# Performance work log

Measured on AMD Instinct MI355X. Metric: run time of the kernel, lower is better.

## Reference

```python
import jax, jax.numpy as jnp
import numpy as np

C = 192; WS = 8; SHIFT = 4; NH = 6; HD = 32; N = WS * WS; EPS = 1e-5


def _cpb_table(ws):
    r = np.arange(-(ws - 1), ws, dtype=np.float32)
    t = np.stack(np.meshgrid(r, r, indexing='ij'), axis=-1) / (ws - 1) * 8.0
    t = np.sign(t) * np.log2(np.abs(t) + 1.0) / np.log2(8.0)
    return t.reshape(-1, 2)  # ((2ws-1)^2, 2)


def _rel_index(ws):
    c = np.stack(np.meshgrid(np.arange(ws), np.arange(ws), indexing='ij')).reshape(2, -1)
    rel = (c[:, :, None] - c[:, None, :]).transpose(1, 2, 0).astype(np.int64)
    rel[..., 0] += ws - 1; rel[..., 1] += ws - 1; rel[..., 0] *= 2 * ws - 1
    return rel.sum(-1)  # (N, N)


def _attn_mask(H, W, ws, shift):
    img = np.zeros((H, W), np.float32); cnt = 0.0
    sl = (slice(0, -ws), slice(-ws, -shift), slice(-shift, None))
    for hs in sl:
        for wsl in sl:
            img[hs, wsl] = cnt; cnt += 1.0
    m = img.reshape(H // ws, ws, W // ws, ws).transpose(0, 2, 1, 3).reshape(-1, ws * ws)
    d = m[:, None, :] - m[:, :, None]
    return np.where(d != 0, -100.0, 0.0).astype(np.float32)  # (nW, N, N)


def _ln(x, g, b):
    mu = jnp.mean(x, -1, keepdims=True)
    var = jnp.mean((x - mu) ** 2, -1, keepdims=True)
    return (x - mu) / jnp.sqrt(var + EPS) * g + b


def setup_inputs() -> dict:
    key = jax.random.key(0)
    ks = jax.random.split(key, 8)
    H = W = 384
    w = lambda k, s: jax.random.normal(k, s, jnp.float32) * 0.05
    return {
        'hidden_states': jax.random.normal(ks[0], (1, H * W, C), jnp.float32),
        'q_w': w(ks[1], (C, C)), 'q_b': jnp.zeros((C,), jnp.float32),
        'k_w': w(ks[2], (C, C)),
        'v_w': w(ks[3], (C, C)), 'v_b': jnp.zeros((C,), jnp.float32),
        'logit_scale': jnp.full((NH, 1, 1), np.log(10.0), jnp.float32),
        'cpb_w1': w(ks[4], (2, 512)), 'cpb_b1': jnp.zeros((512,), jnp.float32),
        'cpb_w2': w(ks[5], (512, NH)),
        'proj_w': w(ks[6], (C, C)), 'proj_b': jnp.zeros((C,), jnp.float32),
        'ln1_g': jnp.ones((C,), jnp.float32), 'ln1_b': jnp.zeros((C,), jnp.float32),
        'fc1_w': w(ks[7], (C, 2 * C)), 'fc1_b': jnp.zeros((2 * C,), jnp.float32),
        'fc2_w': w(jax.random.fold_in(key, 9), (2 * C, C)), 'fc2_b': jnp.zeros((C,), jnp.float32),
        'ln2_g': jnp.ones((C,), jnp.float32), 'ln2_b': jnp.zeros((C,), jnp.float32),
        'height': 384, 'width': 384,
    }


def reference(hidden_states, q_w, q_b, k_w, v_w, v_b, logit_scale, cpb_w1, cpb_b1,
              cpb_w2, proj_w, proj_b, ln1_g, ln1_b, fc1_w, fc1_b, fc2_w, fc2_b,
              ln2_g, ln2_b, height, width):
    B = hidden_states.shape[0]
    shortcut = hidden_states
    x = hidden_states.reshape(B, height, width, C)
    # shift
    x = jnp.roll(x, (-SHIFT, -SHIFT), (1, 2))
    # window partition -> (B*nW, N, C)
    win = x.reshape(B, height // WS, WS, width // WS, WS, C).transpose(0, 1, 3, 2, 4, 5).reshape(-1, N, C)
    q = (win @ q_w + q_b).reshape(-1, N, NH, HD).transpose(0, 2, 1, 3)
    k = (win @ k_w).reshape(-1, N, NH, HD).transpose(0, 2, 1, 3)
    v = (win @ v_w + v_b).reshape(-1, N, NH, HD).transpose(0, 2, 1, 3)
    # cosine attention
    qn = q / jnp.maximum(jnp.linalg.norm(q, axis=-1, keepdims=True), 1e-12)
    kn = k / jnp.maximum(jnp.linalg.norm(k, axis=-1, keepdims=True), 1e-12)
    scale = jnp.exp(jnp.minimum(logit_scale, jnp.log(100.0))).reshape(1, NH, 1, 1)
    scores = jnp.einsum('whnd,whmd->whnm', qn, kn) * scale
    # continuous relative position bias via MLP
    table = jnp.asarray(_cpb_table(WS))
    bias_tab = jax.nn.relu(table @ cpb_w1 + cpb_b1) @ cpb_w2  # (169, NH)
    idx = jnp.asarray(_rel_index(WS)).reshape(-1)
    rpb = bias_tab[idx].reshape(N, N, NH).transpose(2, 0, 1)
    rpb = 16.0 * jax.nn.sigmoid(rpb)
    mask = jnp.asarray(_attn_mask(height, width, WS, SHIFT))  # (nW, N, N)
    # NOTE: source adds the mask twice (faithful reproduction)
    scores = scores + rpb[None] + 2.0 * mask[:, None]
    probs = jax.nn.softmax(scores, -1)
    ctx = jnp.einsum('whnm,whmd->whnd', probs, v).transpose(0, 2, 1, 3).reshape(-1, N, C)
    attn = ctx @ proj_w + proj_b
    # window reverse + unshift
    x = attn.reshape(B, height // WS, width // WS, WS, WS, C).transpose(0, 1, 3, 2, 4, 5).reshape(B, height, width, C)
    x = jnp.roll(x, (SHIFT, SHIFT), (1, 2)).reshape(B, height * width, C)
    # post-norm residual (Swin v2 style)
    h = shortcut + _ln(x, ln1_g, ln1_b)
    mlp = jax.nn.gelu(h @ fc1_w + fc1_b, approximate=False) @ fc2_w + fc2_b
    return h + _ln(mlp, ln2_g, ln2_b)
```

## Files before the change

### kernel.cpp

```cpp
#include <hip/hip_runtime.h>
#include <hip/hip_bf16.h>
#include <math.h>

typedef __hip_bfloat16 bf16;
typedef __attribute__((ext_vector_type(8))) short short8;
typedef __attribute__((ext_vector_type(4))) float floatx4;
typedef unsigned int u32;

#define NTOK 147456
#define IMG 384

__device__ __forceinline__ int gather_row(int m) {
    int gw = m >> 6, t = m & 63;
    int wr = gw / 48, wc = gw - wr * 48;
    int hh = wr * 8 + (t >> 3);
    int ww = wc * 8 + (t & 7);
    int oh = hh + 4; if (oh >= IMG) oh -= IMG;
    int ow = ww + 4; if (ow >= IMG) ow -= IMG;
    return oh * IMG + ow;
}

__device__ __forceinline__ unsigned short f2bu(float f) {
    unsigned u = __float_as_uint(f);
    unsigned r = (u + 0x7fffu + ((u >> 16) & 1u)) >> 16;
    return (unsigned short)r;
}
__device__ __forceinline__ float bu2f(unsigned short u) {
    return __uint_as_float(((unsigned)u) << 16);
}

__device__ __forceinline__ u32 cvt_pk_bf16(float lo, float hi) {
    u32 r;
    asm("v_cvt_pk_bf16_f32 %0, %1, %2" : "=v"(r) : "v"(lo), "v"(hi));
    return r;
}

__device__ __forceinline__ float gelu_fast(float x) {
    const float z = fabsf(x) * 0.70710678118654752f;
    const float t = __builtin_amdgcn_rcpf(fmaf(0.3275911f, z, 1.0f));
    float p = fmaf(1.061405429f, t, -1.453152027f);
    p = fmaf(p, t, 1.421413741f);
    p = fmaf(p, t, -0.284496736f);
    p = fmaf(p, t, 0.254829592f);
    p *= t;
    const float e = __expf(-z * z);
    float erfv = fmaf(-p, e, 1.0f);
    erfv = (x < 0.0f) ? -erfv : erfv;
    return 0.5f * x * (1.0f + erfv);
}

__device__ __forceinline__ void async_copy16(void* lds, const void* g) {
    __builtin_amdgcn_global_load_lds(
        (const __attribute__((address_space(1))) u32*)g,
        (__attribute__((address_space(3))) u32*)lds,
        16, 0, 0);
}


__global__ __launch_bounds__(256)
void conv_pack(const float* __restrict__ hidden, bf16* __restrict__ Apk)
{
    const int cid = blockIdx.x * 256 + threadIdx.x;
    const int mtG = cid / 384;
    const int rest = cid - mtG * 384;
    const int kg = rest >> 4, mm = rest & 15;
    const int tok = mtG * 16 + mm;
    const float* p = hidden + (size_t)gather_row(tok) * 192 + kg * 8;
    const float4 a = *(const float4*)p;
    const float4 b = *(const float4*)(p + 4);
    short8 o;
    o[0] = (short)f2bu(a.x); o[1] = (short)f2bu(a.y);
    o[2] = (short)f2bu(a.z); o[3] = (short)f2bu(a.w);
    o[4] = (short)f2bu(b.x); o[5] = (short)f2bu(b.y);
    o[6] = (short)f2bu(b.z); o[7] = (short)f2bu(b.w);
    *(short8*)(Apk + (size_t)cid * 8) = o;
}

__global__ __launch_bounds__(256)
void pack_w(const float* __restrict__ W, bf16* __restrict__ out, int K, int N)
{
    const int cid = blockIdx.x * 256 + threadIdx.x;
    const int KG = K >> 3;
    const int total = (N >> 4) * KG * 16;
    if (cid >= total) return;
    const int n = cid & 15;
    const int kg = (cid >> 4) % KG;
    const int ntG = (cid >> 4) / KG;
    short8 o;
#pragma unroll
    for (int j = 0; j < 8; ++j)
        o[j] = (short)f2bu(W[(size_t)(kg * 8 + j) * N + ntG * 16 + n]);
    *(short8*)(out + (size_t)cid * 8) = o;
}

__global__ __launch_bounds__(256)
void fuse_bias(const float* __restrict__ qb, const float* __restrict__ vb,
               float* __restrict__ out)
{
    const int t = blockIdx.x * 256 + threadIdx.x;
    if (t >= 576) return;
    out[t] = (t < 192) ? qb[t] : ((t < 384) ? 0.0f : vb[t - 384]);
}

#define EPI_NONE 0
#define EPI_GELU 1

template<int KDIM, bool PACK_OUT, int EPI, int KGOUT, int MW>
__global__ __launch_bounds__(256, MW)
void gemm_mfma(const bf16* __restrict__ Apk, const bf16* __restrict__ Bpk,
               const float* __restrict__ bias, bf16* __restrict__ C, int N)
{
    constexpr int KG = KDIM / 8;
    constexpr int KT = KDIM / 32;
    constexpr int KC = KDIM / 192;
    __shared__ __align__(16) char sB[2][24576];
    const int tid = threadIdx.x;
    const int wave = tid >> 6, lane = tid & 63;
    const int bm = blockIdx.x * 128;
    const int NPo = N / 64;
    const char* Bsrc = (const char*)Bpk;

    short8 areg[2][KT];
    {
        const char* Asrc = (const char*)Apk;
#pragma unroll
        for (int x = 0; x < 2; ++x) {
            const size_t rowb = (size_t)((bm >> 4) + wave * 2 + x) * KG * 256;
#pragma unroll
            for (int kt = 0; kt < KT; ++kt)
                areg[x][kt] = *(const short8*)(Asrc + rowb + (size_t)kt * 1024 + lane * 16);
        }
    }

    auto stage = [&](int npo_, int kc_, int bufp) {
#pragma unroll
        for (int i = 0; i < 6; ++i) {
            const int cid = i * 256 + wave * 64 + lane;
            const int nt = cid / 384, off = cid - nt * 384;
            const char* g = Bsrc + ((size_t)((npo_ * 4 + nt) * KG + kc_ * 24) * 256 + (size_t)off * 16);
            async_copy16(sB[bufp] + (i * 256 + wave * 64) * 16, g);
        }
    };

    stage(0, 0, 0);

    for (int npo = 0; npo < NPo; ++npo) {
        floatx4 acc[8];
#pragma unroll
        for (int f = 0; f < 8; ++f)
            acc[f] = (floatx4){0.f, 0.f, 0.f, 0.f};

#pragma unroll
        for (int kc = 0; kc < KC; ++kc) {
            const int p = npo * KC + kc;
            const int buf = p & 1;
            const bool last = (npo == NPo - 1) && (kc == KC - 1);
            if (!last) {
                if (kc < KC - 1) stage(npo, kc + 1, buf ^ 1);
                else             stage(npo + 1, 0, buf ^ 1);
                if (kc == 0 && npo > 0)
                    asm volatile("s_waitcnt vmcnt(10)" ::: "memory");
                else
                    asm volatile("s_waitcnt vmcnt(6)" ::: "memory");
            } else {
                if (KC == 1) asm volatile("s_waitcnt vmcnt(4)" ::: "memory");
                else         asm volatile("s_waitcnt vmcnt(0)" ::: "memory");
            }
            __builtin_amdgcn_sched_barrier(0);
            asm volatile("s_barrier" ::: "memory");

            char* sb = sB[buf];
#pragma unroll
            for (int kt6 = 0; kt6 < 6; ++kt6) {
                const short8 a0 = areg[0][kc * 6 + kt6];
                const short8 a1 = areg[1][kc * 6 + kt6];
#pragma unroll
                for (int nt = 0; nt < 4; ++nt) {
                    const short8 b = *(const short8*)(sb + nt * 6144 + kt6 * 1024 + lane * 16);
                    acc[nt]     = __builtin_amdgcn_mfma_f32_16x16x32_bf16(a0, b, acc[nt],     0, 0, 0);
                    acc[4 + nt] = __builtin_amdgcn_mfma_f32_16x16x32_bf16(a1, b, acc[4 + nt], 0, 0, 0);
                }
            }
            if (kc < KC - 1)
                asm volatile("s_barrier" ::: "memory");
        }

        {
            const int ebuf = (npo * KC + KC - 1) & 1;
            asm volatile("s_barrier" ::: "memory");
            char* wb = sB[ebuf] + wave * 4608;
#pragma unroll
            for (int m2 = 0; m2 < 2; ++m2) {
#pragma unroll
                for (int nt = 0; nt < 4; ++nt) {
                    const floatx4 v = acc[m2 * 4 + nt];
                    const int c = nt * 16 + (lane & 15);
                    const float bval = bias ? bias[npo * 64 + c] : 0.0f;
#pragma unroll
                    for (int i = 0; i < 4; ++i) {
                        float f = v[i] + bval;
                        if (EPI == EPI_GELU)
                            f = gelu_fast(f);
                        const int r = m2 * 16 + (lane >> 4) * 4 + i;
                        *(unsigned short*)(wb + (r * 72 + c) * 2) = f2bu(f);
                    }
                }
            }
            asm volatile("s_waitcnt lgkmcnt(0)" ::: "memory");
            asm volatile("s_barrier" ::: "memory");
            if (PACK_OUT) {
                const int m = lane >> 1, c2 = (lane & 1) * 32;
                const int grow = bm + wave * 32 + m;
#pragma unroll
                for (int i = 0; i < 4; ++i) {
                    const short8 row = *(const short8*)(wb + (m * 72 + c2 + i * 8) * 2);
                    const int gcol = npo * 64 + c2 + i * 8;
                    bf16* dst = C + ((size_t)((grow >> 4) * KGOUT + (gcol >> 3)) * 16 + (grow & 15)) * 8;
                    *(short8*)dst = row;
                }
            } else {
                const int mr = lane >> 3, c2 = (lane & 7) * 8;
#pragma unroll
                for (int i = 0; i < 4; ++i) {
                    const int rr = i * 8 + mr;
                    const short8 row = *(const short8*)(wb + (rr * 72 + c2) * 2);
                    bf16* dst = C + (size_t)(bm + wave * 32 + rr) * N + npo * 64 + c2;
                    *(short8*)dst = row;
                }
            }
            asm volatile("s_barrier" ::: "memory");
        }
    }
}


__device__ __forceinline__ float cpb_coord(int i) {
    float a = (float)(i - 7) * (8.0f / 7.0f);
    float s = (a > 0.f) ? 1.f : ((a < 0.f) ? -1.f : 0.f);
    return s * log2f(fabsf(a) + 1.0f) * (1.0f / 3.0f);
}

__global__ __launch_bounds__(512)
void cpb_mlp(const float* __restrict__ w1, const float* __restrict__ b1,
             const float* __restrict__ w2, float* __restrict__ tab)
{
    const int r = blockIdx.x;
    const int t = threadIdx.x;
    const float x0 = cpb_coord(r / 15);
    const float x1 = cpb_coord(r % 15);
    const float hgt = fmaxf(x0 * w1[t] + x1 * w1[512 + t] + b1[t], 0.0f);
    __shared__ float red[512];
    for (int n = 0; n < 6; ++n) {
        red[t] = hgt * w2[t * 6 + n];
        __syncthreads();
        for (int s = 256; s > 0; s >>= 1) {
            if (t < s) red[t] += red[t + s];
            __syncthreads();
        }
        if (t == 0) tab[r * 6 + n] = red[0];
        __syncthreads();
    }
}

__global__ __launch_bounds__(256)
void rpb_expand(const float* __restrict__ tab, const float* __restrict__ logit_scale,
                float* __restrict__ rpb)
{
    const int idx = blockIdx.x * 256 + threadIdx.x;
    if (idx >= 6 * 4096) return;
    const int h = idx >> 12;
    const int t = (idx >> 6) & 63;
    const int j = idx & 63;
    const int pr = t >> 3, pc = t & 7, qr = j >> 3, qc = j & 7;
    const int ridx = (pr - qr + 7) * 15 + (pc - qc + 7);
    const float v = tab[ridx * 6 + h];
    const float scale = __expf(fminf(logit_scale[h], 4.6051701859880914f));
    rpb[idx] = 16.0f / (1.0f + expf(-v)) - scale - 16.0f;
}

__global__ __launch_bounds__(256, 2)
void attn_mfma(const bf16* __restrict__ QKV, const float* __restrict__ rpb,
               const float* __restrict__ logit_scale, bf16* __restrict__ Ctx)
{
    __shared__ __align__(16) char lds[4][9216];
    const int wave = threadIdx.x >> 6, lane = threadIdx.x & 63;
    const int l15 = lane & 15, quad = lane >> 4;
    const int wh = blockIdx.x * 4 + wave;
    const int w = wh / 6, h = wh - w * 6;
    char* Pb = lds[wave];
    char* Vt = lds[wave] + 4608;

    const bf16* wbase = QKV + (size_t)w * 64 * 576;

    {
        const bf16* vp = wbase + (size_t)lane * 576 + 384 + h * 32;
        const short8 v0 = *(const short8*)(vp);
        const short8 v1 = *(const short8*)(vp + 8);
        const short8 v2 = *(const short8*)(vp + 16);
        const short8 v3 = *(const short8*)(vp + 24);
#pragma unroll
        for (int j = 0; j < 8; ++j) {
            *(short*)(Vt + ((j     ) * 72 + lane) * 2) = v0[j];
            *(short*)(Vt + ((j +  8) * 72 + lane) * 2) = v1[j];
            *(short*)(Vt + ((j + 16) * 72 + lane) * 2) = v2[j];
            *(short*)(Vt + ((j + 24) * 72 + lane) * 2) = v3[j];
        }
    }

    const int wr = w / 48, wc = w - wr * 48;
    const bool edge = (wr == 47) || (wc == 47);
    int rid_j[4];
    if (edge) {
#pragma unroll
        for (int jt = 0; jt < 4; ++jt) {
            const int t = jt * 16 + l15;
            const int rr = (wr == 47) ? (((t >> 3) < 4) ? 1 : 2) : 0;
            const int rc = (wc == 47) ? (((t & 7) < 4) ? 1 : 2) : 0;
            rid_j[jt] = rr * 3 + rc;
        }
    }

    const float scale = __expf(fminf(logit_scale[h], 4.6051701859880914f));

    short8 kfr[4];
    float rnk[4];
#pragma unroll
    for (int jt = 0; jt < 4; ++jt) {
        kfr[jt] = *(const short8*)(wbase + (size_t)(jt * 16 + l15) * 576 + 192 + h * 32 + quad * 8);
        float ss = 0.f;
#pragma unroll
        for (int j = 0; j < 8; ++j) {
            const float f = bu2f((unsigned short)kfr[jt][j]);
            ss = fmaf(f, f, ss);
        }
        ss += __shfl_xor(ss, 16); ss += __shfl_xor(ss, 32);
        rnk[jt] = __builtin_amdgcn_rcpf(fmaxf(__builtin_amdgcn_sqrtf(ss), 1e-12f));
    }

    floatx4 acc[4][4];
    float rnq[4];
#pragma unroll
    for (int it = 0; it < 4; ++it)
#pragma unroll
        for (int jt = 0; jt < 4; ++jt)
            acc[it][jt] = (floatx4){0.f, 0.f, 0.f, 0.f};
#pragma unroll
    for (int it = 0; it < 4; ++it) {
        const short8 qf = *(const short8*)(wbase + (size_t)(it * 16 + l15) * 576 + h * 32 + quad * 8);
        float ss = 0.f;
#pragma unroll
        for (int j = 0; j < 8; ++j) {
            const float f = bu2f((unsigned short)qf[j]);
            ss = fmaf(f, f, ss);
        }
        ss += __shfl_xor(ss, 16); ss += __shfl_xor(ss, 32);
        rnq[it] = scale * __builtin_amdgcn_rcpf(fmaxf(__builtin_amdgcn_sqrtf(ss), 1e-12f));
#pragma unroll
        for (int jt = 0; jt < 4; ++jt)
            acc[it][jt] = __builtin_amdgcn_mfma_f32_16x16x32_bf16(qf, kfr[jt], acc[it][jt], 0, 0, 0);
    }

    const float* rpbh = rpb + h * 4096;

    float inv[4][4];
#pragma unroll
    for (int it = 0; it < 4; ++it) {
#pragma unroll
        for (int r = 0; r < 4; ++r) {
            const int i = it * 16 + quad * 4 + r;
            const float rq = __shfl(rnq[it], quad * 4 + r);
            int rid_i = 0;
            if (edge) {
                const int rr = (wr == 47) ? (((i >> 3) < 4) ? 1 : 2) : 0;
                const int rc = (wc == 47) ? (((i & 7) < 4) ? 1 : 2) : 0;
                rid_i = rr * 3 + rc;
            }
            float s = 0.f;
#pragma unroll
            for (int jt = 0; jt < 4; ++jt) {
                float v = fmaf(acc[it][jt][r], rq * rnk[jt], rpbh[i * 64 + jt * 16 + l15]);
                if (edge && rid_i != rid_j[jt]) v -= 200.0f;
                const float e = __expf(v);
                acc[it][jt][r] = e; s += e;
            }
            s += __shfl_xor(s, 1); s += __shfl_xor(s, 2);
            s += __shfl_xor(s, 4); s += __shfl_xor(s, 8);
            inv[it][r] = __builtin_amdgcn_rcpf(s);
        }
    }

    floatx4 ctx[4][2];
#pragma unroll
    for (int it = 0; it < 4; ++it)
#pragma unroll
        for (int dt = 0; dt < 2; ++dt)
            ctx[it][dt] = (floatx4){0.f, 0.f, 0.f, 0.f};

#pragma unroll
    for (int ks = 0; ks < 2; ++ks) {
#pragma unroll
        for (int it = 0; it < 4; ++it)
#pragma unroll
            for (int r = 0; r < 4; ++r) {
                const int i = it * 16 + quad * 4 + r;
                const u32 pk = cvt_pk_bf16(acc[it][ks * 2][r], acc[it][ks * 2 + 1][r]);
                *(short*)(Pb + (i * 36 + l15) * 2)      = (short)pk;
                *(short*)(Pb + (i * 36 + 16 + l15) * 2) = (short)(pk >> 16);
            }
#pragma unroll
        for (int it = 0; it < 4; ++it) {
            const short8 pf = *(const short8*)(Pb + ((it * 16 + l15) * 36 + quad * 8) * 2);
#pragma unroll
            for (int dt = 0; dt < 2; ++dt) {
                const short8 vf = *(const short8*)(Vt + ((dt * 16 + l15) * 72 + ks * 32 + quad * 8) * 2);
                ctx[it][dt] = __builtin_amdgcn_mfma_f32_16x16x32_bf16(pf, vf, ctx[it][dt], 0, 0, 0);
            }
        }
    }

#pragma unroll
    for (int it = 0; it < 4; ++it)
#pragma unroll
        for (int r = 0; r < 4; ++r) {
            const int i = it * 16 + quad * 4 + r;
            const u32 pk = cvt_pk_bf16(ctx[it][0][r] * inv[it][r], ctx[it][1][r] * inv[it][r]);
            *(short*)(Pb + (i * 36 + l15) * 2)      = (short)pk;
            *(short*)(Pb + (i * 36 + 16 + l15) * 2) = (short)(pk >> 16);
        }

    const int tok = w * 64 + lane;
    const size_t obase = ((size_t)(tok >> 4) * 24 + h * 4) * 128 + (size_t)(tok & 15) * 8;
#pragma unroll
    for (int c = 0; c < 4; ++c) {
        const short8 row = *(const short8*)(Pb + (lane * 36 + c * 8) * 2);
        *(short8*)(Ctx + obase + (size_t)c * 128) = row;
    }
}


__global__ __launch_bounds__(256)
void ln_h(const bf16* __restrict__ X, const float* __restrict__ hidden,
          const float* __restrict__ g, const float* __restrict__ b,
          bf16* __restrict__ Hres, bf16* __restrict__ Hpk)
{
    const int lane = threadIdx.x & 63;
    const int wv = threadIdx.x >> 6;
    const int tok = blockIdx.x * 4 + wv;
    const int grow = gather_row(tok);
    __shared__ float rows[4][192];
    const bf16* xr = X + (size_t)tok * 192;
    const float x0 = bu2f(*(const unsigned short*)(xr + lane));
    const float x1 = bu2f(*(const unsigned short*)(xr + lane + 64));
    const float x2 = bu2f(*(const unsigned short*)(xr + lane + 128));
    float s = x0 + x1 + x2;
#pragma unroll
    for (int o = 32; o > 0; o >>= 1) s += __shfl_xor(s, o);
    const float mean = s * (1.0f / 192.0f);
    const float d0 = x0 - mean, d1 = x1 - mean, d2 = x2 - mean;
    float vsum = d0 * d0 + d1 * d1 + d2 * d2;
#pragma unroll
    for (int o = 32; o > 0; o >>= 1) vsum += __shfl_xor(vsum, o);
    const float rstd = rsqrtf(vsum * (1.0f / 192.0f) + 1e-5f);
    const float* hr = hidden + (size_t)grow * 192;
    const float h0 = hr[lane]       + d0 * rstd * g[lane]       + b[lane];
    const float h1 = hr[lane + 64]  + d1 * rstd * g[lane + 64]  + b[lane + 64];
    const float h2 = hr[lane + 128] + d2 * rstd * g[lane + 128] + b[lane + 128];
    bf16* hres = Hres + (size_t)tok * 192;
    *(unsigned short*)(hres + lane)       = f2bu(h0);
    *(unsigned short*)(hres + lane + 64)  = f2bu(h1);
    *(unsigned short*)(hres + lane + 128) = f2bu(h2);
    rows[wv][lane] = h0; rows[wv][lane + 64] = h1; rows[wv][lane + 128] = h2;
    __syncthreads();
    if (lane < 24) {
        short8 o;
#pragma unroll
        for (int j = 0; j < 8; ++j) o[j] = (short)f2bu(rows[wv][lane * 8 + j]);
        const int mtG = tok >> 4, mm = tok & 15;
        *(short8*)(Hpk + ((size_t)(mtG * 24 + lane) * 16 + mm) * 8) = o;
    }
}

__global__ __launch_bounds__(256)
void ln_out(const bf16* __restrict__ Y, const bf16* __restrict__ Hres,
            const float* __restrict__ g, const float* __restrict__ b,
            float* __restrict__ Out)
{
    const int lane = threadIdx.x & 63;
    const int tok = blockIdx.x * 4 + (threadIdx.x >> 6);
    const int grow = gather_row(tok);
    const bf16* yr = Y + (size_t)tok * 192;
    const float x0 = bu2f(*(const unsigned short*)(yr + lane));
    const float x1 = bu2f(*(const unsigned short*)(yr + lane + 64));
    const float x2 = bu2f(*(const unsigned short*)(yr + lane + 128));
    float s = x0 + x1 + x2;
#pragma unroll
    for (int o = 32; o > 0; o >>= 1) s += __shfl_xor(s, o);
    const float mean = s * (1.0f / 192.0f);
    const float d0 = x0 - mean, d1 = x1 - mean, d2 = x2 - mean;
    float vsum = d0 * d0 + d1 * d1 + d2 * d2;
#pragma unroll
    for (int o = 32; o > 0; o >>= 1) vsum += __shfl_xor(vsum, o);
    const float rstd = rsqrtf(vsum * (1.0f / 192.0f) + 1e-5f);
    const bf16* hr = Hres + (size_t)tok * 192;
    float* op = Out + (size_t)grow * 192;
    op[lane]       = bu2f(*(const unsigned short*)(hr + lane))       + d0 * rstd * g[lane]       + b[lane];
    op[lane + 64]  = bu2f(*(const unsigned short*)(hr + lane + 64))  + d1 * rstd * g[lane + 64]  + b[lane + 64];
    op[lane + 128] = bu2f(*(const unsigned short*)(hr + lane + 128)) + d2 * rstd * g[lane + 128] + b[lane + 128];
}


extern "C" void kernel_launch(void* const* d_in, const int* in_sizes, int n_in,
                              void* d_out, int out_size, void* d_ws, size_t ws_size,
                              hipStream_t stream)
{
    const float* hidden = (const float*)d_in[0];
    const float* q_w = (const float*)d_in[1];
    const float* q_b = (const float*)d_in[2];
    const float* k_w = (const float*)d_in[3];
    const float* v_w = (const float*)d_in[4];
    const float* v_b = (const float*)d_in[5];
    const float* logit_scale = (const float*)d_in[6];
    const float* cpb_w1 = (const float*)d_in[7];
    const float* cpb_b1 = (const float*)d_in[8];
    const float* cpb_w2 = (const float*)d_in[9];
    const float* proj_w = (const float*)d_in[10];
    const float* proj_b = (const float*)d_in[11];
    const float* ln1_g = (const float*)d_in[12];
    const float* ln1_b = (const float*)d_in[13];
    const float* fc1_w = (const float*)d_in[14];
    const float* fc1_b = (const float*)d_in[15];
    const float* fc2_w = (const float*)d_in[16];
    const float* fc2_b = (const float*)d_in[17];
    const float* ln2_g = (const float*)d_in[18];
    const float* ln2_b = (const float*)d_in[19];

    char* ws = (char*)d_ws;
    bf16*  APK   = (bf16*)(ws + 0);
    float* RPB   = (float*)(ws + 0);
    bf16*  PROJW = (bf16*)(ws + (1 << 20));
    bf16*  MID   = (bf16*)(ws + 0);
    bf16*  CTX   = (bf16*)(ws + 56623104);
    bf16*  QKVW  = (bf16*)(ws + 56623104);
    float* QKVB  = (float*)(ws + 56844288);
    float* TAB   = (float*)(ws + 56846592);
    bf16*  QKV   = (bf16*)(ws + 113246208);
    bf16*  HRES  = (bf16*)(ws + 113246208);
    bf16*  HPK   = (bf16*)(ws + 169869312);
    bf16*  Y     = (bf16*)(ws + 226492416);
    bf16*  X     = (bf16*)(ws + 283115520);
    bf16*  FC1W  = (bf16*)(ws + 283115520);
    bf16*  FC2W  = (bf16*)(ws + 283262976);
    float* OUT   = (float*)d_out;

    cpb_mlp<<<225, 512, 0, stream>>>(cpb_w1, cpb_b1, cpb_w2, TAB);
    fuse_bias<<<3, 256, 0, stream>>>(q_b, v_b, QKVB);
    pack_w<<<18, 256, 0, stream>>>(q_w, QKVW,                 192, 192);
    pack_w<<<18, 256, 0, stream>>>(k_w, QKVW + 12 * 24 * 128, 192, 192);
    pack_w<<<18, 256, 0, stream>>>(v_w, QKVW + 24 * 24 * 128, 192, 192);
    conv_pack<<<13824, 256, 0, stream>>>(hidden, APK);

    gemm_mfma<192, false, EPI_NONE, 1, 3><<<1152, 256, 0, stream>>>(APK, QKVW, QKVB, QKV, 576);

    rpb_expand<<<96, 256, 0, stream>>>(TAB, logit_scale, RPB);
    pack_w<<<18, 256, 0, stream>>>(proj_w, PROJW, 192, 192);

    attn_mfma<<<3456, 256, 0, stream>>>(QKV, RPB, logit_scale, CTX);

    gemm_mfma<192, false, EPI_NONE, 1, 3><<<1152, 256, 0, stream>>>(CTX, PROJW, proj_b, X, 192);

    ln_h<<<NTOK / 4, 256, 0, stream>>>(X, hidden, ln1_g, ln1_b, HRES, HPK);

    pack_w<<<36, 256, 0, stream>>>(fc1_w, FC1W, 192, 384);
    pack_w<<<36, 256, 0, stream>>>(fc2_w, FC2W, 384, 192);

    gemm_mfma<192, true, EPI_GELU, 48, 3><<<1152, 256, 0, stream>>>(HPK, FC1W, fc1_b, MID, 384);
    gemm_mfma<384, false, EPI_NONE, 1, 2><<<1152, 256, 0, stream>>>(MID, FC2W, fc2_b, Y, 192);

    ln_out<<<NTOK / 4, 256, 0, stream>>>(Y, HRES, ln2_g, ln2_b, OUT);
}
```

Baseline: 670.0 us.

## Load GEMM B fragments directly from global memory instead of LDS staging

The GEMM kernel drops the double-buffered async global-to-LDS staging of the packed B matrix, along with its s_waitcnt and barrier choreography. Each wave now reads its B fragments straight from global memory (via cache) into registers for the MFMAs. The output epilogue uses a small private per-wave LDS buffer, so no block-wide barriers remain. This removes synchronisation and cuts LDS use, which may raise occupancy. The cost is that B reuse across waves now relies on the L1/L2 caches, and global load latency is exposed with no explicit prefetch.

```diff
diff --git a/kernel.cpp b/kernel.cpp
--- a/kernel.cpp
+++ b/kernel.cpp
@@ -47,13 +47,6 @@
     float erfv = fmaf(-p, e, 1.0f);
     erfv = (x < 0.0f) ? -erfv : erfv;
     return 0.5f * x * (1.0f + erfv);
-}
-
-__device__ __forceinline__ void async_copy16(void* lds, const void* g) {
-    __builtin_amdgcn_global_load_lds(
-        (const __attribute__((address_space(1))) u32*)g,
-        (__attribute__((address_space(3))) u32*)lds,
-        16, 0, 0);
 }
 
 
@@ -112,13 +105,12 @@
 {
     constexpr int KG = KDIM / 8;
     constexpr int KT = KDIM / 32;
-    constexpr int KC = KDIM / 192;
-    __shared__ __align__(16) char sB[2][24576];
-    const int tid = threadIdx.x;
-    const int wave = tid >> 6, lane = tid & 63;
+    __shared__ __align__(16) char wbs[4][4608];
+    const int wave = threadIdx.x >> 6, lane = threadIdx.x & 63;
     const int bm = blockIdx.x * 128;
     const int NPo = N / 64;
     const char* Bsrc = (const char*)Bpk;
+    char* wb = wbs[wave];
 
     short8 areg[2][KT];
     {
@@ -132,103 +124,61 @@
         }
     }
 
-    auto stage = [&](int npo_, int kc_, int bufp) {
-#pragma unroll
-        for (int i = 0; i < 6; ++i) {
-            const int cid = i * 256 + wave * 64 + lane;
-            const int nt = cid / 384, off = cid - nt * 384;
-            const char* g = Bsrc + ((size_t)((npo_ * 4 + nt) * KG + kc_ * 24) * 256 + (size_t)off * 16);
-            async_copy16(sB[bufp] + (i * 256 + wave * 64) * 16, g);
-        }
-    };
-
-    stage(0, 0, 0);
-
     for (int npo = 0; npo < NPo; ++npo) {
         floatx4 acc[8];
 #pragma unroll
         for (int f = 0; f < 8; ++f)
             acc[f] = (floatx4){0.f, 0.f, 0.f, 0.f};
 
-#pragma unroll
-        for (int kc = 0; kc < KC; ++kc) {
-            const int p = npo * KC + kc;
-            const int buf = p & 1;
-            const bool last = (npo == NPo - 1) && (kc == KC - 1);
-            if (!last) {
-                if (kc < KC - 1) stage(npo, kc + 1, buf ^ 1);
-                else             stage(npo + 1, 0, buf ^ 1);
-                if (kc == 0 && npo > 0)
-                    asm volatile("s_waitcnt vmcnt(10)" ::: "memory");
-                else
-                    asm volatile("s_waitcnt vmcnt(6)" ::: "memory");
-            } else {
-                if (KC == 1) asm volatile("s_waitcnt vmcnt(4)" ::: "memory");
-                else         asm volatile("s_waitcnt vmcnt(0)" ::: "memory");
-            }
-            __builtin_amdgcn_sched_barrier(0);
-            asm volatile("s_barrier" ::: "memory");
-
-            char* sb = sB[buf];
-#pragma unroll
-            for (int kt6 = 0; kt6 < 6; ++kt6) {
-                const short8 a0 = areg[0][kc * 6 + kt6];
-                const short8 a1 = areg[1][kc * 6 + kt6];
-#pragma unroll
-                for (int nt = 0; nt < 4; ++nt) {
-                    const short8 b = *(const short8*)(sb + nt * 6144 + kt6 * 1024 + lane * 16);
-                    acc[nt]     = __builtin_amdgcn_mfma_f32_16x16x32_bf16(a0, b, acc[nt],     0, 0, 0);
-                    acc[4 + nt] = __builtin_amdgcn_mfma_f32_16x16x32_bf16(a1, b, acc[4 + nt], 0, 0, 0);
+        const char* bbase = Bsrc + (size_t)npo * 4 * KG * 256 + lane * 16;
+#pragma unroll
+        for (int kt = 0; kt < KT; ++kt) {
+            const short8 a0 = areg[0][kt];
+            const short8 a1 = areg[1][kt];
+#pragma unroll
+            for (int nt = 0; nt < 4; ++nt) {
+                const short8 b = *(const short8*)(bbase + (size_t)(nt * KG + kt * 4) * 256);
+                acc[nt]     = __builtin_amdgcn_mfma_f32_16x16x32_bf16(a0, b, acc[nt],     0, 0, 0);
+                acc[4 + nt] = __builtin_amdgcn_mfma_f32_16x16x32_bf16(a1, b, acc[4 + nt], 0, 0, 0);
+            }
+        }
+
+#pragma unroll
+        for (int m2 = 0; m2 < 2; ++m2) {
+#pragma unroll
+            for (int nt = 0; nt < 4; ++nt) {
+                const floatx4 v = acc[m2 * 4 + nt];
+                const int c = nt * 16 + (lane & 15);
+                const float bval = bias ? bias[npo * 64 + c] : 0.0f;
+#pragma unroll
+                for (int i = 0; i < 4; ++i) {
+                    float f = v[i] + bval;
+                    if (EPI == EPI_GELU)
+                        f = gelu_fast(f);
+                    const int r = m2 * 16 + (lane >> 4) * 4 + i;
+                    *(unsigned short*)(wb + (r * 72 + c) * 2) = f2bu(f);
                 }
             }
-            if (kc < KC - 1)
-                asm volatile("s_barrier" ::: "memory");
-        }
-
-        {
-            const int ebuf = (npo * KC + KC - 1) & 1;
-            asm volatile("s_barrier" ::: "memory");
-            char* wb = sB[ebuf] + wave * 4608;
-#pragma unroll
-            for (int m2 = 0; m2 < 2; ++m2) {
-#pragma unroll
-                for (int nt = 0; nt < 4; ++nt) {
-                    const floatx4 v = acc[m2 * 4 + nt];
-                    const int c = nt * 16 + (lane & 15);
-                    const float bval = bias ? bias[npo * 64 + c] : 0.0f;
-#pragma unroll
-                    for (int i = 0; i < 4; ++i) {
-                        float f = v[i] + bval;
-                        if (EPI == EPI_GELU)
-                            f = gelu_fast(f);
-                        const int r = m2 * 16 + (lane >> 4) * 4 + i;
-                        *(unsigned short*)(wb + (r * 72 + c) * 2) = f2bu(f);
-                    }
-                }
-            }
-            asm volatile("s_waitcnt lgkmcnt(0)" ::: "memory");
-            asm volatile("s_barrier" ::: "memory");
-            if (PACK_OUT) {
-                const int m = lane >> 1, c2 = (lane & 1) * 32;
-                const int grow = bm + wave * 32 + m;
-#pragma unroll
-                for (int i = 0; i < 4; ++i) {
-                    const short8 row = *(const short8*)(wb + (m * 72 + c2 + i * 8) * 2);
-                    const int gcol = npo * 64 + c2 + i * 8;
-                    bf16* dst = C + ((size_t)((grow >> 4) * KGOUT + (gcol >> 3)) * 16 + (grow & 15)) * 8;
-                    *(short8*)dst = row;
-                }
-            } else {
-                const int mr = lane >> 3, c2 = (lane & 7) * 8;
-#pragma unroll
-                for (int i = 0; i < 4; ++i) {
-                    const int rr = i * 8 + mr;
-                    const short8 row = *(const short8*)(wb + (rr * 72 + c2) * 2);
-                    bf16* dst = C + (size_t)(bm + wave * 32 + rr) * N + npo * 64 + c2;
-                    *(short8*)dst = row;
-                }
-            }
-            asm volatile("s_barrier" ::: "memory");
+        }
+        if (PACK_OUT) {
+            const int m = lane >> 1, c2 = (lane & 1) * 32;
+            const int grow = bm + wave * 32 + m;
+#pragma unroll
+            for (int i = 0; i < 4; ++i) {
+                const short8 row = *(const short8*)(wb + (m * 72 + c2 + i * 8) * 2);
+                const int gcol = npo * 64 + c2 + i * 8;
+                bf16* dst = C + ((size_t)((grow >> 4) * KGOUT + (gcol >> 3)) * 16 + (grow & 15)) * 8;
+                *(short8*)dst = row;
+            }
+        } else {
+            const int mr = lane >> 3, c2 = (lane & 7) * 8;
+#pragma unroll
+            for (int i = 0; i < 4; ++i) {
+                const int rr = i * 8 + mr;
+                const short8 row = *(const short8*)(wb + (rr * 72 + c2) * 2);
+                bf16* dst = C + (size_t)(bm + wave * 32 + rr) * N + npo * 64 + c2;
+                *(short8*)dst = row;
+            }
         }
     }
 }
```

Result: slower. 763.5 us (+13.9%).
